# Performance work log

Hardware: AMD Instinct MI355X
Metric: run time of the kernel (lower is better)

The kernel has to match this reference:

```python
import jax, jax.numpy as jnp
import numpy as np

B, F, CIN, COUT, K, R = 128, 1024, 16, 16, 4, 2


def setup_inputs() -> dict:
    key = jax.random.key(0)
    k1, k2 = jax.random.split(key)
    ll = jax.random.normal(k1, (B, F, CIN, R), dtype=jnp.float32)
    logits = jax.random.normal(k2, (COUT, CIN, K, K, R), dtype=jnp.float32)
    return {"ll": ll, "logits": logits, "kernel_size": K}


def reference(ll, logits, kernel_size):
    # ll: (B, F, Cin, R); logits: (O, Cin, K, K, R)
    b, f, cin, r = ll.shape
    o = logits.shape[0]
    k = kernel_size
    h = w = int(round(f ** 0.5))
    hb, wb = h // k, w // k
    # normalize weights over input channels (sum_dim=1)
    log_w = jax.nn.log_softmax(logits, axis=1)          # (O, Cin, K, K, R)
    # im2col-like patch reshape: (B, Cin, hb, wb, K, K, R)
    x = jnp.transpose(ll, (0, 2, 1, 3)).reshape(b, cin, hb, k, wb, k, r)
    x = jnp.transpose(x, (0, 1, 2, 4, 3, 5, 6))
    # broadcast-add log weights per kernel position, reduce over Cin
    w_b = log_w[None, :, :, None, None, :, :, :]        # (1, O, Cin, 1, 1, K, K, R)
    out = jax.nn.logsumexp(x[:, None] + w_b, axis=2)    # (B, O, hb, wb, K, K, R)
    # reassemble spatial grid and flatten back to features
    out = jnp.transpose(out, (0, 1, 2, 4, 3, 5, 6)).reshape(b, o, h, w, r)
    out = out.reshape(b, o, f, r)
    return jnp.transpose(out, (0, 2, 1, 3))             # (B, F, O, R)
```

## Files before the change

kernel.cpp:

```cpp
#include <hip/hip_runtime.h>


#define LDS_STRIDE 520

__global__ __launch_bounds__(256) void sumconv_fused(
    const float* __restrict__ ll, const float* __restrict__ logits,
    float* __restrict__ out) {
  __shared__ float sw[16 * LDS_STRIDE];

  const int tid = threadIdx.x;

  for (int s = tid; s < 512; s += 256) {
    const int r = s & 1, kk = (s >> 1) & 15, o = s >> 5;
    float v[16];
    float m = -1e30f;
#pragma unroll
    for (int ci = 0; ci < 16; ++ci) {
      v[ci] = logits[((o * 16 + ci) * 16 + kk) * 2 + r];
      m = fmaxf(m, v[ci]);
    }
    float sum = 0.f;
#pragma unroll
    for (int ci = 0; ci < 16; ++ci) {
      v[ci] = __expf(v[ci] - m);
      sum += v[ci];
    }
    const float inv = 1.0f / sum;
#pragma unroll
    for (int ci = 0; ci < 16; ++ci)
      sw[kk * LDS_STRIDE + (o * 16 + ci) * 2 + r] = v[ci] * inv;
  }
  __syncthreads();

  const int i = blockIdx.x * 256 + tid;
  const int f = i & 1023;
  const int kk = (((f >> 5) & 3) << 2) | (f & 3);
  const float* __restrict__ wbase = sw + kk * LDS_STRIDE;

  const float4* __restrict__ inp = (const float4*)(ll + (size_t)i * 32);
  float E[32];
#pragma unroll
  for (int j = 0; j < 8; ++j) {
    float4 v = inp[j];
    E[4 * j + 0] = __expf(v.x);
    E[4 * j + 1] = __expf(v.y);
    E[4 * j + 2] = __expf(v.z);
    E[4 * j + 3] = __expf(v.w);
  }

  float4* __restrict__ op = (float4*)(out + (size_t)i * 32);
#pragma unroll 1
  for (int o = 0; o < 16; o += 2) {
    float a00 = 0.f, a01 = 0.f, a10 = 0.f, a11 = 0.f;
#pragma unroll
    for (int ci = 0; ci < 16; ++ci) {
      const float2 w0 = *(const float2*)(wbase + (o * 16 + ci) * 2);
      const float2 w1 = *(const float2*)(wbase + ((o + 1) * 16 + ci) * 2);
      a00 = fmaf(w0.x, E[2 * ci + 0], a00);
      a01 = fmaf(w0.y, E[2 * ci + 1], a01);
      a10 = fmaf(w1.x, E[2 * ci + 0], a10);
      a11 = fmaf(w1.y, E[2 * ci + 1], a11);
    }
    op[o >> 1] = make_float4(__logf(a00), __logf(a01), __logf(a10), __logf(a11));
  }
}

extern "C" void kernel_launch(void* const* d_in, const int* in_sizes, int n_in,
                              void* d_out, int out_size, void* d_ws, size_t ws_size,
                              hipStream_t stream) {
  const float* ll     = (const float*)d_in[0];
  const float* logits = (const float*)d_in[1];
  float* out = (float*)d_out;
  sumconv_fused<<<512, 256, 0, stream>>>(ll, logits, out);
}
```

Before: 16.63 us.

## Split each pixel's outputs across four threads with LDS-staged exponentials

```diff
diff --git a/kernel.cpp b/kernel.cpp
--- a/kernel.cpp
+++ b/kernel.cpp
@@ -1,22 +1,30 @@
 #include <hip/hip_runtime.h>
 
 
-#define LDS_STRIDE 520
+#define WSTRIDE 520
+#define ESTRIDE 36
 
-__global__ __launch_bounds__(256) void sumconv_fused(
+__global__ __launch_bounds__(256, 4) void sumconv_fused(
     const float* __restrict__ ll, const float* __restrict__ logits,
     float* __restrict__ out) {
-  __shared__ float sw[16 * LDS_STRIDE];
+  __shared__ float sw[8 * WSTRIDE + 64 * ESTRIDE];
+  float* __restrict__ swW = sw;
+  float* __restrict__ swE = sw + 8 * WSTRIDE;
 
   const int tid = threadIdx.x;
+  const int blk = blockIdx.x;
+  const int f_base = (blk * 64) & 1023;
+  const int kkbase = ((f_base >> 5) & 3) * 4;
 
-  for (int s = tid; s < 512; s += 256) {
-    const int r = s & 1, kk = (s >> 1) & 15, o = s >> 5;
+  {
+    const int r = tid & 1, kkloc = (tid >> 1) & 7, o = tid >> 4;
+    const int kk = kkbase + kkloc;
+    const float* __restrict__ lg = logits + o * 512 + kk * 2 + r;
     float v[16];
     float m = -1e30f;
 #pragma unroll
     for (int ci = 0; ci < 16; ++ci) {
-      v[ci] = logits[((o * 16 + ci) * 16 + kk) * 2 + r];
+      v[ci] = lg[ci * 32];
       m = fmaxf(m, v[ci]);
     }
     float sum = 0.f;
@@ -28,40 +36,47 @@
     const float inv = 1.0f / sum;
 #pragma unroll
     for (int ci = 0; ci < 16; ++ci)
-      sw[kk * LDS_STRIDE + (o * 16 + ci) * 2 + r] = v[ci] * inv;
+      swW[kkloc * WSTRIDE + ci * 32 + o * 2 + r] = v[ci] * inv;
+  }
+
+  {
+    const float4* __restrict__ src = (const float4*)(ll + (size_t)blk * 2048);
+#pragma unroll
+    for (int j = 0; j < 2; ++j) {
+      const int p = tid + 256 * j;
+      const float4 v = src[p];
+      const int row = p >> 3, c4 = p & 7;
+      *(float4*)(swE + row * ESTRIDE + c4 * 4) =
+          make_float4(__expf(v.x), __expf(v.y), __expf(v.z), __expf(v.w));
+    }
   }
   __syncthreads();
 
-  const int i = blockIdx.x * 256 + tid;
+  const int row = tid >> 2, q = tid & 3;
+  const int i = blk * 64 + row;
   const int f = i & 1023;
   const int kk = (((f >> 5) & 3) << 2) | (f & 3);
-  const float* __restrict__ wbase = sw + kk * LDS_STRIDE;
+  const float* __restrict__ wb = swW + (kk & 7) * WSTRIDE + q * 4;
+  const float* __restrict__ eb = swE + row * ESTRIDE;
 
-  const float4* __restrict__ inp = (const float4*)(ll + (size_t)i * 32);
-  float E[32];
+  float Ef[32];
 #pragma unroll
-  for (int j = 0; j < 8; ++j) {
-    float4 v = inp[j];
-    E[4 * j + 0] = __expf(v.x);
-    E[4 * j + 1] = __expf(v.y);
-    E[4 * j + 2] = __expf(v.z);
-    E[4 * j + 3] = __expf(v.w);
-  }
+  for (int k = 0; k < 8; ++k)
+    *(float4*)(Ef + 4 * k) = *(const float4*)(eb + 4 * k);
 
   float4* __restrict__ op = (float4*)(out + (size_t)i * 32);
 #pragma unroll 1
-  for (int o = 0; o < 16; o += 2) {
+  for (int oo = 0; oo < 2; ++oo) {
     float a00 = 0.f, a01 = 0.f, a10 = 0.f, a11 = 0.f;
 #pragma unroll
     for (int ci = 0; ci < 16; ++ci) {
-      const float2 w0 = *(const float2*)(wbase + (o * 16 + ci) * 2);
-      const float2 w1 = *(const float2*)(wbase + ((o + 1) * 16 + ci) * 2);
-      a00 = fmaf(w0.x, E[2 * ci + 0], a00);
-      a01 = fmaf(w0.y, E[2 * ci + 1], a01);
-      a10 = fmaf(w1.x, E[2 * ci + 0], a10);
-      a11 = fmaf(w1.y, E[2 * ci + 1], a11);
+      const float4 w = *(const float4*)(wb + ci * 32 + oo * 16);
+      a00 = fmaf(w.x, Ef[2 * ci + 0], a00);
+      a01 = fmaf(w.y, Ef[2 * ci + 1], a01);
+      a10 = fmaf(w.z, Ef[2 * ci + 0], a10);
+      a11 = fmaf(w.w, Ef[2 * ci + 1], a11);
     }
-    op[o >> 1] = make_float4(__logf(a00), __logf(a01), __logf(a10), __logf(a11));
+    op[q + 4 * oo] = make_float4(__logf(a00), __logf(a01), __logf(a10), __logf(a11));
   }
 }
 
@@ -71,5 +86,5 @@
   const float* ll     = (const float*)d_in[0];
   const float* logits = (const float*)d_in[1];
   float* out = (float*)d_out;
-  sumconv_fused<<<512, 256, 0, stream>>>(ll, logits, out);
+  sumconv_fused<<<2048, 256, 0, stream>>>(ll, logits, out);
 }
```

Result: faster. 15.13 us (-9.1%).

## Assign one kernel position per block and split output channels across thread pairs

Applied to the files above, without the earlier changes.

```diff
diff --git a/kernel.cpp b/kernel.cpp
--- a/kernel.cpp
+++ b/kernel.cpp
@@ -1,22 +1,36 @@
 #include <hip/hip_runtime.h>
 
 
-#define LDS_STRIDE 520
-
-__global__ __launch_bounds__(256) void sumconv_fused(
+__global__ __launch_bounds__(256, 4) void sumconv_fused(
     const float* __restrict__ ll, const float* __restrict__ logits,
     float* __restrict__ out) {
-  __shared__ float sw[16 * LDS_STRIDE];
+  __shared__ float wlds[1024];
 
   const int tid = threadIdx.x;
+  const int blk = blockIdx.x;
+  const int kk = blk >> 6;
+  const int s  = blk & 63;
+  const int ki = kk >> 2, kj = kk & 3;
 
-  for (int s = tid; s < 512; s += 256) {
-    const int r = s & 1, kk = (s >> 1) & 15, o = s >> 5;
+  const int rp = s * 128 + (tid >> 1);
+  const int bb = rp >> 6;
+  const int cd = rp & 63;
+  const int f  = 128 * (cd >> 3) + 32 * ki + 4 * (cd & 7) + kj;
+  const int h  = tid & 1;
+
+  const float4* __restrict__ src = (const float4*)(ll + ((size_t)bb * 1024 + f) * 32);
+  float4 L[8];
+#pragma unroll
+  for (int j = 0; j < 8; ++j) L[j] = src[j];
+
+  if (tid < 32) {
+    const int o = tid >> 1, r = tid & 1;
+    const float* __restrict__ lg = logits + o * 512 + kk * 2 + r;
     float v[16];
     float m = -1e30f;
 #pragma unroll
     for (int ci = 0; ci < 16; ++ci) {
-      v[ci] = logits[((o * 16 + ci) * 16 + kk) * 2 + r];
+      v[ci] = lg[ci * 32];
       m = fmaxf(m, v[ci]);
     }
     float sum = 0.f;
@@ -28,40 +42,34 @@
     const float inv = 1.0f / sum;
 #pragma unroll
     for (int ci = 0; ci < 16; ++ci)
-      sw[kk * LDS_STRIDE + (o * 16 + ci) * 2 + r] = v[ci] * inv;
+      wlds[(o >> 1) * 64 + ci * 4 + (o & 1) * 2 + r] = v[ci] * inv;
   }
-  __syncthreads();
+  asm volatile("s_waitcnt lgkmcnt(0)" ::: "memory");
+  __builtin_amdgcn_s_barrier();
 
-  const int i = blockIdx.x * 256 + tid;
-  const int f = i & 1023;
-  const int kk = (((f >> 5) & 3) << 2) | (f & 3);
-  const float* __restrict__ wbase = sw + kk * LDS_STRIDE;
-
-  const float4* __restrict__ inp = (const float4*)(ll + (size_t)i * 32);
   float E[32];
 #pragma unroll
   for (int j = 0; j < 8; ++j) {
-    float4 v = inp[j];
-    E[4 * j + 0] = __expf(v.x);
-    E[4 * j + 1] = __expf(v.y);
-    E[4 * j + 2] = __expf(v.z);
-    E[4 * j + 3] = __expf(v.w);
+    E[4 * j + 0] = __expf(L[j].x);
+    E[4 * j + 1] = __expf(L[j].y);
+    E[4 * j + 2] = __expf(L[j].z);
+    E[4 * j + 3] = __expf(L[j].w);
   }
 
-  float4* __restrict__ op = (float4*)(out + (size_t)i * 32);
-#pragma unroll 1
-  for (int o = 0; o < 16; o += 2) {
+  float4* __restrict__ op = (float4*)(out + ((size_t)bb * 1024 + f) * 32);
+#pragma unroll
+  for (int pp = 0; pp < 4; ++pp) {
+    const float* __restrict__ wp = wlds + (4 * h + pp) * 64;
     float a00 = 0.f, a01 = 0.f, a10 = 0.f, a11 = 0.f;
 #pragma unroll
     for (int ci = 0; ci < 16; ++ci) {
-      const float2 w0 = *(const float2*)(wbase + (o * 16 + ci) * 2);
-      const float2 w1 = *(const float2*)(wbase + ((o + 1) * 16 + ci) * 2);
-      a00 = fmaf(w0.x, E[2 * ci + 0], a00);
-      a01 = fmaf(w0.y, E[2 * ci + 1], a01);
-      a10 = fmaf(w1.x, E[2 * ci + 0], a10);
-      a11 = fmaf(w1.y, E[2 * ci + 1], a11);
+      const float4 w = *(const float4*)(wp + ci * 4);
+      a00 = fmaf(w.x, E[2 * ci + 0], a00);
+      a01 = fmaf(w.y, E[2 * ci + 1], a01);
+      a10 = fmaf(w.z, E[2 * ci + 0], a10);
+      a11 = fmaf(w.w, E[2 * ci + 1], a11);
     }
-    op[o >> 1] = make_float4(__logf(a00), __logf(a01), __logf(a10), __logf(a11));
+    op[4 * h + pp] = make_float4(__logf(a00), __logf(a01), __logf(a10), __logf(a11));
   }
 }
 
@@ -71,5 +79,5 @@
   const float* ll     = (const float*)d_in[0];
   const float* logits = (const float*)d_in[1];
   float* out = (float*)d_out;
-  sumconv_fused<<<512, 256, 0, stream>>>(ll, logits, out);
+  sumconv_fused<<<1024, 256, 0, stream>>>(ll, logits, out);
 }
```

New measurement: 15.46 us. 7.1% less time.
